# Kernel tuning notes

Measured on AMD Instinct MI355X. Metric: run time of the kernel, lower is better.

## Reference

```python
import jax, jax.numpy as jnp
import numpy as np

N = 100000

def gcn_conv(x, edge_index, W, b):
    # PyG GCNConv: add self-loops, symmetric norm D^-1/2 (A+I) D^-1/2, then aggregate x@W
    n = x.shape[0]
    loops = jnp.arange(n, dtype=edge_index.dtype)
    row = jnp.concatenate([edge_index[0], loops])  # source
    col = jnp.concatenate([edge_index[1], loops])  # target
    deg = jax.ops.segment_sum(jnp.ones_like(col, dtype=x.dtype), col, num_segments=n)
    dinv = jnp.where(deg > 0, jax.lax.rsqrt(deg), 0.0)
    norm = dinv[row] * dinv[col]            # [E+N]
    xw = x @ W                               # transform first (smaller message dim)
    msg = xw[row] * norm[:, None]            # gather + normalize
    out = jax.ops.segment_sum(msg, col, num_segments=n)  # scatter-add
    return out + b

def setup_inputs() -> dict:
    key = jax.random.key(0)
    k1, k2, k3, k4, k5, k6 = jax.random.split(key, 6)
    F_in, H, C = 512, 256, 40
    x = jax.random.normal(k1, (N, F_in), dtype=jnp.float32)
    edge_index = jax.random.randint(k2, (2, 3200000), 0, N, dtype=jnp.int64)
    W1 = jax.random.normal(k3, (F_in, H), dtype=jnp.float32) / np.sqrt(F_in)
    b1 = jnp.zeros((H,), dtype=jnp.float32)
    W2 = jax.random.normal(k4, (H, C), dtype=jnp.float32) / np.sqrt(H)
    b2 = jnp.zeros((C,), dtype=jnp.float32)
    return {"x": x, "edge_index": edge_index, "W1": W1, "b1": b1, "W2": W2, "b2": b2}

def reference(x, edge_index, W1, b1, W2, b2):
    h = gcn_conv(x, edge_index, W1, b1)
    h = jax.nn.relu(h)
    # dropout skipped (eval mode / training=False)
    h = gcn_conv(h, edge_index, W2, b2)
    return jax.nn.log_softmax(h, axis=1)
```

## Files before the change

### kernel.cpp

```cpp
#include <hip/hip_runtime.h>
#include <math.h>

typedef __attribute__((ext_vector_type(8))) short short8;
typedef __attribute__((ext_vector_type(4))) float f32x4;

static __device__ __forceinline__ unsigned short f2bf(float f) {
    unsigned int u = __float_as_uint(f);
    unsigned int r = (u + 0x7FFFu + ((u >> 16) & 1u)) >> 16;
    return (unsigned short)r;
}
static __device__ __forceinline__ float b2f(unsigned short s) {
    return __uint_as_float(((unsigned int)s) << 16);
}


__global__ void count_kernel(const int* __restrict__ ei, int* __restrict__ cnt, int E) {
    int e = blockIdx.x * 256 + threadIdx.x;
    if (e < E) atomicAdd(&cnt[ei[E + e]], 1);
}

__global__ void scanA_kernel(const int* __restrict__ cnt, float* __restrict__ dinv,
                             int* __restrict__ colptr, int* __restrict__ bsum, int n) {
    __shared__ int s[256];
    int b = blockIdx.x, t = threadIdx.x;
    int i = b * 512 + 2 * t;
    int c0 = (i     < n) ? cnt[i]     : 0;
    int c1 = (i + 1 < n) ? cnt[i + 1] : 0;
    if (i     < n) dinv[i]     = rsqrtf((float)(c0 + 1));
    if (i + 1 < n) dinv[i + 1] = rsqrtf((float)(c1 + 1));
    int v = c0 + c1;
    s[t] = v;
    __syncthreads();
    #pragma unroll
    for (int o = 1; o < 256; o <<= 1) {
        int x = (t >= o) ? s[t - o] : 0;
        __syncthreads();
        s[t] += x;
        __syncthreads();
    }
    int excl = s[t] - v;
    if (i     < n) colptr[i]     = excl;
    if (i + 1 < n) colptr[i + 1] = excl + c0;
    if (t == 255) bsum[b] = s[t];
}

__global__ void scanB_kernel(int* bsum, int nb) {
    __shared__ int s[256];
    int t = threadIdx.x;
    int v = (t < nb) ? bsum[t] : 0;
    s[t] = v;
    __syncthreads();
    #pragma unroll
    for (int o = 1; o < 256; o <<= 1) {
        int x = (t >= o) ? s[t - o] : 0;
        __syncthreads();
        s[t] += x;
        __syncthreads();
    }
    if (t < nb) bsum[t] = s[t] - v;
}

__global__ void scanC_kernel(int* __restrict__ colptr, const int* __restrict__ bsum,
                             int n, int E) {
    int b = blockIdx.x, t = threadIdx.x;
    int off = bsum[b];
    int i = b * 512 + 2 * t;
    if (i     < n) colptr[i]     += off;
    if (i + 1 < n) colptr[i + 1] += off;
    if (b == 0 && t == 0) colptr[n] = E;
}

__global__ void fill_kernel(const int* __restrict__ ei, const int* __restrict__ colptr,
                            int* __restrict__ fillc, int* __restrict__ eidx, int E) {
    int e = blockIdx.x * 256 + threadIdx.x;
    if (e < E) {
        int r = ei[e];
        int c = ei[E + e];
        int pos = colptr[c] + atomicAdd(&fillc[c], 1);
        eidx[pos] = r;
    }
}

__global__ void convert_w1_kernel(const float* __restrict__ W1, unsigned short* __restrict__ w1t) {
    int id = blockIdx.x * 256 + threadIdx.x;
    int k = id >> 8, n = id & 255;
    w1t[(size_t)n * 512 + k] = f2bf(W1[id]);
}


__global__ __launch_bounds__(256) void gemm1_kernel(const float* __restrict__ x,
                                                    const unsigned short* __restrict__ w1t,
                                                    const float* __restrict__ dinv,
                                                    unsigned short* __restrict__ xs, int M) {
    __shared__ unsigned short As[64 * 40];
    __shared__ unsigned short Bs[256 * 40];
    int t = threadIdx.x;
    int m0 = blockIdx.x * 64;
    int lane = t & 63, wv = t >> 6;
    int wn = wv * 64;
    int lm = lane & 15, q = lane >> 4;

    int ra = t >> 2, kc = (t & 3) * 8;
    int am = m0 + ra; if (am >= M) am = M - 1;
    const float* Ap = x + (size_t)am * 512 + kc;
    const unsigned short* Bp = w1t + (size_t)ra * 512 + kc;

    f32x4 acc[4][4];
    f32x4 z = {0.f, 0.f, 0.f, 0.f};
    #pragma unroll
    for (int i = 0; i < 4; i++)
        #pragma unroll
        for (int j = 0; j < 4; j++) acc[i][j] = z;

    for (int k0 = 0; k0 < 512; k0 += 32) {
        float4 a0 = *(const float4*)(Ap + k0);
        float4 a1 = *(const float4*)(Ap + k0 + 4);
        uint4 b0 = *(const uint4*)(Bp + k0);
        uint4 b1 = *(const uint4*)(Bp + k0 + 64 * 512);
        uint4 b2 = *(const uint4*)(Bp + k0 + 128 * 512);
        uint4 b3 = *(const uint4*)(Bp + k0 + 192 * 512);
        __syncthreads();
        uint4 ap;
        ap.x = (unsigned int)f2bf(a0.x) | ((unsigned int)f2bf(a0.y) << 16);
        ap.y = (unsigned int)f2bf(a0.z) | ((unsigned int)f2bf(a0.w) << 16);
        ap.z = (unsigned int)f2bf(a1.x) | ((unsigned int)f2bf(a1.y) << 16);
        ap.w = (unsigned int)f2bf(a1.z) | ((unsigned int)f2bf(a1.w) << 16);
        *(uint4*)&As[ra * 40 + kc] = ap;
        *(uint4*)&Bs[(ra +   0) * 40 + kc] = b0;
        *(uint4*)&Bs[(ra +  64) * 40 + kc] = b1;
        *(uint4*)&Bs[(ra + 128) * 40 + kc] = b2;
        *(uint4*)&Bs[(ra + 192) * 40 + kc] = b3;
        __syncthreads();
        short8 af[4], bfr[4];
        #pragma unroll
        for (int i = 0; i < 4; i++)
            af[i] = *(const short8*)&As[(i * 16 + lm) * 40 + q * 8];
        #pragma unroll
        for (int j = 0; j < 4; j++)
            bfr[j] = *(const short8*)&Bs[(wn + j * 16 + lm) * 40 + q * 8];
        #pragma unroll
        for (int i = 0; i < 4; i++)
            #pragma unroll
            for (int j = 0; j < 4; j++)
                acc[i][j] = __builtin_amdgcn_mfma_f32_16x16x32_bf16(af[i], bfr[j], acc[i][j], 0, 0, 0);
    }

    #pragma unroll
    for (int i = 0; i < 4; i++) {
        #pragma unroll
        for (int r = 0; r < 4; r++) {
            int m = m0 + i * 16 + q * 4 + r;
            if (m < M) {
                float d = dinv[m];
                #pragma unroll
                for (int j = 0; j < 4; j++) {
                    int n = wn + j * 16 + lm;
                    xs[(size_t)m * 256 + n] = f2bf(acc[i][j][r] * d);
                }
            }
        }
    }
}


__global__ __launch_bounds__(256) void spmm1_kernel(const unsigned short* __restrict__ xs,
                                                    const int* __restrict__ colptr,
                                                    const int* __restrict__ eidx,
                                                    const float* __restrict__ dinv,
                                                    const float* __restrict__ b1,
                                                    unsigned short* __restrict__ h, int Nn) {
    int wid = threadIdx.x >> 6, lane = threadIdx.x & 63;
    int c = blockIdx.x * 4 + wid;
    if (c >= Nn) return;
    const uint2* base = (const uint2*)xs;
    uint2 sv = base[(size_t)c * 64 + lane];
    float a0 = __uint_as_float(sv.x << 16);
    float a1 = __uint_as_float(sv.x & 0xFFFF0000u);
    float a2 = __uint_as_float(sv.y << 16);
    float a3 = __uint_as_float(sv.y & 0xFFFF0000u);
    int j = colptr[c], jend = colptr[c + 1];
    for (; j + 7 < jend; j += 8) {
        uint2 v0 = base[(size_t)eidx[j    ] * 64 + lane];
        uint2 v1 = base[(size_t)eidx[j + 1] * 64 + lane];
        uint2 v2 = base[(size_t)eidx[j + 2] * 64 + lane];
        uint2 v3 = base[(size_t)eidx[j + 3] * 64 + lane];
        uint2 v4 = base[(size_t)eidx[j + 4] * 64 + lane];
        uint2 v5 = base[(size_t)eidx[j + 5] * 64 + lane];
        uint2 v6 = base[(size_t)eidx[j + 6] * 64 + lane];
        uint2 v7 = base[(size_t)eidx[j + 7] * 64 + lane];
        a0 += __uint_as_float(v0.x << 16) + __uint_as_float(v1.x << 16)
            + __uint_as_float(v2.x << 16) + __uint_as_float(v3.x << 16)
            + __uint_as_float(v4.x << 16) + __uint_as_float(v5.x << 16)
            + __uint_as_float(v6.x << 16) + __uint_as_float(v7.x << 16);
        a1 += __uint_as_float(v0.x & 0xFFFF0000u) + __uint_as_float(v1.x & 0xFFFF0000u)
            + __uint_as_float(v2.x & 0xFFFF0000u) + __uint_as_float(v3.x & 0xFFFF0000u)
            + __uint_as_float(v4.x & 0xFFFF0000u) + __uint_as_float(v5.x & 0xFFFF0000u)
            + __uint_as_float(v6.x & 0xFFFF0000u) + __uint_as_float(v7.x & 0xFFFF0000u);
        a2 += __uint_as_float(v0.y << 16) + __uint_as_float(v1.y << 16)
            + __uint_as_float(v2.y << 16) + __uint_as_float(v3.y << 16)
            + __uint_as_float(v4.y << 16) + __uint_as_float(v5.y << 16)
            + __uint_as_float(v6.y << 16) + __uint_as_float(v7.y << 16);
        a3 += __uint_as_float(v0.y & 0xFFFF0000u) + __uint_as_float(v1.y & 0xFFFF0000u)
            + __uint_as_float(v2.y & 0xFFFF0000u) + __uint_as_float(v3.y & 0xFFFF0000u)
            + __uint_as_float(v4.y & 0xFFFF0000u) + __uint_as_float(v5.y & 0xFFFF0000u)
            + __uint_as_float(v6.y & 0xFFFF0000u) + __uint_as_float(v7.y & 0xFFFF0000u);
    }
    for (; j < jend; j++) {
        uint2 v0 = base[(size_t)eidx[j] * 64 + lane];
        a0 += __uint_as_float(v0.x << 16);
        a1 += __uint_as_float(v0.x & 0xFFFF0000u);
        a2 += __uint_as_float(v0.y << 16);
        a3 += __uint_as_float(v0.y & 0xFFFF0000u);
    }
    float d = dinv[c];
    float4 bb = ((const float4*)b1)[lane];
    float f0 = fmaxf(a0 * d + bb.x, 0.f);
    float f1 = fmaxf(a1 * d + bb.y, 0.f);
    float f2 = fmaxf(a2 * d + bb.z, 0.f);
    float f3 = fmaxf(a3 * d + bb.w, 0.f);
    uint2 p;
    p.x = (unsigned int)f2bf(f0) | ((unsigned int)f2bf(f1) << 16);
    p.y = (unsigned int)f2bf(f2) | ((unsigned int)f2bf(f3) << 16);
    *(uint2*)(h + (size_t)c * 256 + 4 * lane) = p;
}


__global__ __launch_bounds__(320) void gemm2_kernel(const unsigned short* __restrict__ h,
                                                    const float* __restrict__ W2,
                                                    const float* __restrict__ dinv,
                                                    unsigned short* __restrict__ t2p, int M) {
    __shared__ float w2s[256 * 40];
    __shared__ float hs[32][260];
    int t = threadIdx.x;
    for (int idx = t; idx < 10240; idx += 320) w2s[idx] = W2[idx];
    int r0g = blockIdx.x * 32;
    for (int idx = t; idx < 2048; idx += 320) {
        int rr = idx >> 6, k4 = (idx & 63) * 4;
        int row = r0g + rr;
        float4 v = make_float4(0.f, 0.f, 0.f, 0.f);
        if (row < M) {
            uint2 u = *(const uint2*)(h + (size_t)row * 256 + k4);
            v.x = __uint_as_float(u.x << 16);
            v.y = __uint_as_float(u.x & 0xFFFF0000u);
            v.z = __uint_as_float(u.y << 16);
            v.w = __uint_as_float(u.y & 0xFFFF0000u);
        }
        *(float4*)&hs[rr][k4] = v;
    }
    __syncthreads();
    int c = t % 40, rb = (t / 40) * 4;
    float a0 = 0.f, a1 = 0.f, a2 = 0.f, a3 = 0.f;
    #pragma unroll 2
    for (int k = 0; k < 256; k += 4) {
        float4 h0 = *(const float4*)&hs[rb + 0][k];
        float4 h1 = *(const float4*)&hs[rb + 1][k];
        float4 h2 = *(const float4*)&hs[rb + 2][k];
        float4 h3 = *(const float4*)&hs[rb + 3][k];
        float w0 = w2s[(k + 0) * 40 + c];
        float w1 = w2s[(k + 1) * 40 + c];
        float w2 = w2s[(k + 2) * 40 + c];
        float w3 = w2s[(k + 3) * 40 + c];
        a0 += h0.x * w0 + h0.y * w1 + h0.z * w2 + h0.w * w3;
        a1 += h1.x * w0 + h1.y * w1 + h1.z * w2 + h1.w * w3;
        a2 += h2.x * w0 + h2.y * w1 + h2.z * w2 + h2.w * w3;
        a3 += h3.x * w0 + h3.y * w1 + h3.z * w2 + h3.w * w3;
    }
    int row = r0g + rb;
    if (row + 0 < M) t2p[(size_t)(row + 0) * 64 + c] = f2bf(a0 * dinv[row + 0]);
    if (row + 1 < M) t2p[(size_t)(row + 1) * 64 + c] = f2bf(a1 * dinv[row + 1]);
    if (row + 2 < M) t2p[(size_t)(row + 2) * 64 + c] = f2bf(a2 * dinv[row + 2]);
    if (row + 3 < M) t2p[(size_t)(row + 3) * 64 + c] = f2bf(a3 * dinv[row + 3]);
}


__global__ __launch_bounds__(256) void spmm2_kernel(const unsigned short* __restrict__ t2p,
                                                    const int* __restrict__ colptr,
                                                    const int* __restrict__ eidx,
                                                    const float* __restrict__ dinv,
                                                    const float* __restrict__ b2,
                                                    float* __restrict__ out, int Nn) {
    int wid = threadIdx.x >> 6, lane = threadIdx.x & 63;
    int c = blockIdx.x * 4 + wid;
    if (c >= Nn) return;
    float acc = b2f(t2p[(size_t)c * 64 + lane]);
    int j = colptr[c], jend = colptr[c + 1];
    float a0 = 0.f, a1 = 0.f, a2 = 0.f, a3 = 0.f;
    for (; j + 7 < jend; j += 8) {
        float u0 = b2f(t2p[(size_t)eidx[j    ] * 64 + lane]);
        float u1 = b2f(t2p[(size_t)eidx[j + 1] * 64 + lane]);
        float u2 = b2f(t2p[(size_t)eidx[j + 2] * 64 + lane]);
        float u3 = b2f(t2p[(size_t)eidx[j + 3] * 64 + lane]);
        float u4 = b2f(t2p[(size_t)eidx[j + 4] * 64 + lane]);
        float u5 = b2f(t2p[(size_t)eidx[j + 5] * 64 + lane]);
        float u6 = b2f(t2p[(size_t)eidx[j + 6] * 64 + lane]);
        float u7 = b2f(t2p[(size_t)eidx[j + 7] * 64 + lane]);
        a0 += u0 + u4; a1 += u1 + u5; a2 += u2 + u6; a3 += u3 + u7;
    }
    for (; j < jend; j++) a0 += b2f(t2p[(size_t)eidx[j] * 64 + lane]);
    acc += (a0 + a1) + (a2 + a3);
    float val = (lane < 40) ? (acc * dinv[c] + b2[lane]) : -INFINITY;
    float m = val;
    #pragma unroll
    for (int o = 32; o > 0; o >>= 1) { float z = __shfl_xor(m, o); m = fmaxf(m, z); }
    float ex = (lane < 40) ? expf(val - m) : 0.f;
    float s = ex;
    #pragma unroll
    for (int o = 32; o > 0; o >>= 1) s += __shfl_xor(s, o);
    if (lane < 40) out[(size_t)c * 40 + lane] = val - m - logf(s);
}


extern "C" void kernel_launch(void* const* d_in, const int* in_sizes, int n_in,
                              void* d_out, int out_size, void* d_ws, size_t ws_size,
                              hipStream_t stream) {
    const float* x  = (const float*)d_in[0];
    const int*   ei = (const int*)d_in[1];
    const float* W1 = (const float*)d_in[2];
    const float* b1 = (const float*)d_in[3];
    const float* W2 = (const float*)d_in[4];
    const float* b2 = (const float*)d_in[5];
    float* out = (float*)d_out;

    int N = in_sizes[0] / 512;
    int E = in_sizes[1] / 2;

    char* p = (char*)d_ws;
    auto carve = [&](size_t bytes) -> char* {
        char* q = p;
        p += (bytes + 1023) & ~(size_t)1023;
        return q;
    };
    float* dinv   = (float*)carve((size_t)N * 4);
    int*   cnt    = (int*)carve((size_t)N * 4);
    int*   colptr = (int*)carve(((size_t)N + 1) * 4);
    int*   fillc  = (int*)carve((size_t)N * 4);
    int*   bsum   = (int*)carve(1024 * 4);
    int*   eidx   = (int*)carve((size_t)E * 4);
    unsigned short* w1t = (unsigned short*)carve((size_t)256 * 512 * 2);
    unsigned short* xs  = (unsigned short*)carve((size_t)N * 256 * 2);
    unsigned short* h   = (unsigned short*)carve((size_t)N * 256 * 2);
    unsigned short* t2p = (unsigned short*)carve((size_t)N * 64 * 2);

    hipMemsetAsync(cnt,   0, (size_t)N * 4, stream);
    hipMemsetAsync(fillc, 0, (size_t)N * 4, stream);

    int eb = (E + 255) / 256;
    int nb = (N + 511) / 512;

    count_kernel<<<eb, 256, 0, stream>>>(ei, cnt, E);
    scanA_kernel<<<nb, 256, 0, stream>>>(cnt, dinv, colptr, bsum, N);
    scanB_kernel<<<1, 256, 0, stream>>>(bsum, nb);
    scanC_kernel<<<nb, 256, 0, stream>>>(colptr, bsum, N, E);
    fill_kernel<<<eb, 256, 0, stream>>>(ei, colptr, fillc, eidx, E);
    convert_w1_kernel<<<512, 256, 0, stream>>>(W1, w1t);

    int mb = (N + 63) / 64;
    gemm1_kernel<<<mb, 256, 0, stream>>>(x, w1t, dinv, xs, N);
    spmm1_kernel<<<(N + 3) / 4, 256, 0, stream>>>(xs, colptr, eidx, dinv, b1, h, N);
    gemm2_kernel<<<(N + 31) / 32, 320, 0, stream>>>(h, W2, dinv, t2p, N);
    spmm2_kernel<<<(N + 3) / 4, 256, 0, stream>>>(t2p, colptr, eidx, dinv, b2, out, N);
}
```

Measured before the change: 1.050 ms.

## Use MFMA for second GEMM, double-buffer first GEMM, shrink SpMM unroll

Measured after the change: 949.2 us. 9.6% less time.

```diff
diff --git a/kernel.cpp b/kernel.cpp
--- a/kernel.cpp
+++ b/kernel.cpp
@@ -81,10 +81,19 @@
     }
 }
 
-__global__ void convert_w1_kernel(const float* __restrict__ W1, unsigned short* __restrict__ w1t) {
+__global__ void prep_w_kernel(const float* __restrict__ W1, const float* __restrict__ W2,
+                              unsigned short* __restrict__ w1t, unsigned short* __restrict__ w2t) {
     int id = blockIdx.x * 256 + threadIdx.x;
-    int k = id >> 8, n = id & 255;
-    w1t[(size_t)n * 512 + k] = f2bf(W1[id]);
+    if (id < 512 * 256) {
+        int k = id >> 8, n = id & 255;
+        w1t[(size_t)n * 512 + k] = f2bf(W1[id]);
+    } else {
+        int id2 = id - 512 * 256;
+        if (id2 < 64 * 256) {
+            int n = id2 >> 8, k = id2 & 255;
+            w2t[id2] = (n < 40) ? f2bf(W2[k * 40 + n]) : (unsigned short)0;
+        }
+    }
 }
 
 
@@ -92,8 +101,8 @@
                                                     const unsigned short* __restrict__ w1t,
                                                     const float* __restrict__ dinv,
                                                     unsigned short* __restrict__ xs, int M) {
-    __shared__ unsigned short As[64 * 40];
-    __shared__ unsigned short Bs[256 * 40];
+    __shared__ unsigned short As[2][64 * 40];
+    __shared__ unsigned short Bs[2][256 * 40];
     int t = threadIdx.x;
     int m0 = blockIdx.x * 64;
     int lane = t & 63, wv = t >> 6;
@@ -112,37 +121,64 @@
         #pragma unroll
         for (int j = 0; j < 4; j++) acc[i][j] = z;
 
-    for (int k0 = 0; k0 < 512; k0 += 32) {
-        float4 a0 = *(const float4*)(Ap + k0);
-        float4 a1 = *(const float4*)(Ap + k0 + 4);
-        uint4 b0 = *(const uint4*)(Bp + k0);
-        uint4 b1 = *(const uint4*)(Bp + k0 + 64 * 512);
-        uint4 b2 = *(const uint4*)(Bp + k0 + 128 * 512);
-        uint4 b3 = *(const uint4*)(Bp + k0 + 192 * 512);
-        __syncthreads();
+    float4 a0 = *(const float4*)(Ap + 0);
+    float4 a1 = *(const float4*)(Ap + 4);
+    uint4 b0 = *(const uint4*)(Bp + 0);
+    uint4 b1 = *(const uint4*)(Bp + 64 * 512);
+    uint4 b2 = *(const uint4*)(Bp + 128 * 512);
+    uint4 b3 = *(const uint4*)(Bp + 192 * 512);
+    {
         uint4 ap;
         ap.x = (unsigned int)f2bf(a0.x) | ((unsigned int)f2bf(a0.y) << 16);
         ap.y = (unsigned int)f2bf(a0.z) | ((unsigned int)f2bf(a0.w) << 16);
         ap.z = (unsigned int)f2bf(a1.x) | ((unsigned int)f2bf(a1.y) << 16);
         ap.w = (unsigned int)f2bf(a1.z) | ((unsigned int)f2bf(a1.w) << 16);
-        *(uint4*)&As[ra * 40 + kc] = ap;
-        *(uint4*)&Bs[(ra +   0) * 40 + kc] = b0;
-        *(uint4*)&Bs[(ra +  64) * 40 + kc] = b1;
-        *(uint4*)&Bs[(ra + 128) * 40 + kc] = b2;
-        *(uint4*)&Bs[(ra + 192) * 40 + kc] = b3;
-        __syncthreads();
+        *(uint4*)&As[0][ra * 40 + kc] = ap;
+        *(uint4*)&Bs[0][(ra +   0) * 40 + kc] = b0;
+        *(uint4*)&Bs[0][(ra +  64) * 40 + kc] = b1;
+        *(uint4*)&Bs[0][(ra + 128) * 40 + kc] = b2;
+        *(uint4*)&Bs[0][(ra + 192) * 40 + kc] = b3;
+    }
+    __syncthreads();
+
+    int buf = 0;
+    for (int k0 = 0; k0 < 512; k0 += 32) {
+        bool more = (k0 + 32) < 512;
+        if (more) {
+            a0 = *(const float4*)(Ap + k0 + 32);
+            a1 = *(const float4*)(Ap + k0 + 36);
+            b0 = *(const uint4*)(Bp + k0 + 32);
+            b1 = *(const uint4*)(Bp + k0 + 32 + 64 * 512);
+            b2 = *(const uint4*)(Bp + k0 + 32 + 128 * 512);
+            b3 = *(const uint4*)(Bp + k0 + 32 + 192 * 512);
+        }
         short8 af[4], bfr[4];
         #pragma unroll
         for (int i = 0; i < 4; i++)
-            af[i] = *(const short8*)&As[(i * 16 + lm) * 40 + q * 8];
+            af[i] = *(const short8*)&As[buf][(i * 16 + lm) * 40 + q * 8];
         #pragma unroll
         for (int j = 0; j < 4; j++)
-            bfr[j] = *(const short8*)&Bs[(wn + j * 16 + lm) * 40 + q * 8];
+            bfr[j] = *(const short8*)&Bs[buf][(wn + j * 16 + lm) * 40 + q * 8];
         #pragma unroll
         for (int i = 0; i < 4; i++)
             #pragma unroll
             for (int j = 0; j < 4; j++)
                 acc[i][j] = __builtin_amdgcn_mfma_f32_16x16x32_bf16(af[i], bfr[j], acc[i][j], 0, 0, 0);
+        if (more) {
+            uint4 ap;
+            ap.x = (unsigned int)f2bf(a0.x) | ((unsigned int)f2bf(a0.y) << 16);
+            ap.y = (unsigned int)f2bf(a0.z) | ((unsigned int)f2bf(a0.w) << 16);
+            ap.z = (unsigned int)f2bf(a1.x) | ((unsigned int)f2bf(a1.y) << 16);
+            ap.w = (unsigned int)f2bf(a1.z) | ((unsigned int)f2bf(a1.w) << 16);
+            int nb = buf ^ 1;
+            *(uint4*)&As[nb][ra * 40 + kc] = ap;
+            *(uint4*)&Bs[nb][(ra +   0) * 40 + kc] = b0;
+            *(uint4*)&Bs[nb][(ra +  64) * 40 + kc] = b1;
+            *(uint4*)&Bs[nb][(ra + 128) * 40 + kc] = b2;
+            *(uint4*)&Bs[nb][(ra + 192) * 40 + kc] = b3;
+            __syncthreads();
+        }
+        buf ^= 1;
     }
 
     #pragma unroll
@@ -179,31 +215,19 @@
     float a2 = __uint_as_float(sv.y << 16);
     float a3 = __uint_as_float(sv.y & 0xFFFF0000u);
     int j = colptr[c], jend = colptr[c + 1];
-    for (; j + 7 < jend; j += 8) {
+    for (; j + 3 < jend; j += 4) {
         uint2 v0 = base[(size_t)eidx[j    ] * 64 + lane];
         uint2 v1 = base[(size_t)eidx[j + 1] * 64 + lane];
         uint2 v2 = base[(size_t)eidx[j + 2] * 64 + lane];
         uint2 v3 = base[(size_t)eidx[j + 3] * 64 + lane];
-        uint2 v4 = base[(size_t)eidx[j + 4] * 64 + lane];
-        uint2 v5 = base[(size_t)eidx[j + 5] * 64 + lane];
-        uint2 v6 = base[(size_t)eidx[j + 6] * 64 + lane];
-        uint2 v7 = base[(size_t)eidx[j + 7] * 64 + lane];
         a0 += __uint_as_float(v0.x << 16) + __uint_as_float(v1.x << 16)
-            + __uint_as_float(v2.x << 16) + __uint_as_float(v3.x << 16)
-            + __uint_as_float(v4.x << 16) + __uint_as_float(v5.x << 16)
-            + __uint_as_float(v6.x << 16) + __uint_as_float(v7.x << 16);
+            + __uint_as_float(v2.x << 16) + __uint_as_float(v3.x << 16);
         a1 += __uint_as_float(v0.x & 0xFFFF0000u) + __uint_as_float(v1.x & 0xFFFF0000u)
-            + __uint_as_float(v2.x & 0xFFFF0000u) + __uint_as_float(v3.x & 0xFFFF0000u)
-            + __uint_as_float(v4.x & 0xFFFF0000u) + __uint_as_float(v5.x & 0xFFFF0000u)
-            + __uint_as_float(v6.x & 0xFFFF0000u) + __uint_as_float(v7.x & 0xFFFF0000u);
+            + __uint_as_float(v2.x & 0xFFFF0000u) + __uint_as_float(v3.x & 0xFFFF0000u);
         a2 += __uint_as_float(v0.y << 16) + __uint_as_float(v1.y << 16)
-            + __uint_as_float(v2.y << 16) + __uint_as_float(v3.y << 16)
-            + __uint_as_float(v4.y << 16) + __uint_as_float(v5.y << 16)
-            + __uint_as_float(v6.y << 16) + __uint_as_float(v7.y << 16);
+            + __uint_as_float(v2.y << 16) + __uint_as_float(v3.y << 16);
         a3 += __uint_as_float(v0.y & 0xFFFF0000u) + __uint_as_float(v1.y & 0xFFFF0000u)
-            + __uint_as_float(v2.y & 0xFFFF0000u) + __uint_as_float(v3.y & 0xFFFF0000u)
-            + __uint_as_float(v4.y & 0xFFFF0000u) + __uint_as_float(v5.y & 0xFFFF0000u)
-            + __uint_as_float(v6.y & 0xFFFF0000u) + __uint_as_float(v7.y & 0xFFFF0000u);
+            + __uint_as_float(v2.y & 0xFFFF0000u) + __uint_as_float(v3.y & 0xFFFF0000u);
     }
     for (; j < jend; j++) {
         uint2 v0 = base[(size_t)eidx[j] * 64 + lane];
@@ -225,51 +249,54 @@
 }
 
 
-__global__ __launch_bounds__(320) void gemm2_kernel(const unsigned short* __restrict__ h,
-                                                    const float* __restrict__ W2,
+__global__ __launch_bounds__(256) void gemm2_kernel(const unsigned short* __restrict__ h,
+                                                    const unsigned short* __restrict__ w2t,
                                                     const float* __restrict__ dinv,
                                                     unsigned short* __restrict__ t2p, int M) {
-    __shared__ float w2s[256 * 40];
-    __shared__ float hs[32][260];
+    __shared__ unsigned short As[64 * 264];
+    __shared__ unsigned short Bs[64 * 264];
     int t = threadIdx.x;
-    for (int idx = t; idx < 10240; idx += 320) w2s[idx] = W2[idx];
-    int r0g = blockIdx.x * 32;
-    for (int idx = t; idx < 2048; idx += 320) {
-        int rr = idx >> 6, k4 = (idx & 63) * 4;
-        int row = r0g + rr;
-        float4 v = make_float4(0.f, 0.f, 0.f, 0.f);
-        if (row < M) {
-            uint2 u = *(const uint2*)(h + (size_t)row * 256 + k4);
-            v.x = __uint_as_float(u.x << 16);
-            v.y = __uint_as_float(u.x & 0xFFFF0000u);
-            v.z = __uint_as_float(u.y << 16);
-            v.w = __uint_as_float(u.y & 0xFFFF0000u);
-        }
-        *(float4*)&hs[rr][k4] = v;
+    int m0 = blockIdx.x * 64;
+    int lane = t & 63, wv = t >> 6;
+    int lm = lane & 15, q = lane >> 4;
+
+    #pragma unroll
+    for (int i = 0; i < 8; i++) {
+        int c = t + i * 256;
+        int row = c >> 5, col = (c & 31) * 8;
+        int m = m0 + row; if (m >= M) m = M - 1;
+        uint4 av = *(const uint4*)(h + (size_t)m * 256 + col);
+        *(uint4*)&As[row * 264 + col] = av;
+        uint4 bv = *(const uint4*)(w2t + (size_t)row * 256 + col);
+        *(uint4*)&Bs[row * 264 + col] = bv;
     }
     __syncthreads();
-    int c = t % 40, rb = (t / 40) * 4;
-    float a0 = 0.f, a1 = 0.f, a2 = 0.f, a3 = 0.f;
-    #pragma unroll 2
-    for (int k = 0; k < 256; k += 4) {
-        float4 h0 = *(const float4*)&hs[rb + 0][k];
-        float4 h1 = *(const float4*)&hs[rb + 1][k];
-        float4 h2 = *(const float4*)&hs[rb + 2][k];
-        float4 h3 = *(const float4*)&hs[rb + 3][k];
-        float w0 = w2s[(k + 0) * 40 + c];
-        float w1 = w2s[(k + 1) * 40 + c];
-        float w2 = w2s[(k + 2) * 40 + c];
-        float w3 = w2s[(k + 3) * 40 + c];
-        a0 += h0.x * w0 + h0.y * w1 + h0.z * w2 + h0.w * w3;
-        a1 += h1.x * w0 + h1.y * w1 + h1.z * w2 + h1.w * w3;
-        a2 += h2.x * w0 + h2.y * w1 + h2.z * w2 + h2.w * w3;
-        a3 += h3.x * w0 + h3.y * w1 + h3.z * w2 + h3.w * w3;
-    }
-    int row = r0g + rb;
-    if (row + 0 < M) t2p[(size_t)(row + 0) * 64 + c] = f2bf(a0 * dinv[row + 0]);
-    if (row + 1 < M) t2p[(size_t)(row + 1) * 64 + c] = f2bf(a1 * dinv[row + 1]);
-    if (row + 2 < M) t2p[(size_t)(row + 2) * 64 + c] = f2bf(a2 * dinv[row + 2]);
-    if (row + 3 < M) t2p[(size_t)(row + 3) * 64 + c] = f2bf(a3 * dinv[row + 3]);
+
+    f32x4 acc[4];
+    f32x4 z = {0.f, 0.f, 0.f, 0.f};
+    #pragma unroll
+    for (int j = 0; j < 4; j++) acc[j] = z;
+
+    #pragma unroll
+    for (int k0 = 0; k0 < 256; k0 += 32) {
+        short8 af = *(const short8*)&As[(wv * 16 + lm) * 264 + k0 + q * 8];
+        #pragma unroll
+        for (int j = 0; j < 4; j++) {
+            short8 bf = *(const short8*)&Bs[(j * 16 + lm) * 264 + k0 + q * 8];
+            acc[j] = __builtin_amdgcn_mfma_f32_16x16x32_bf16(af, bf, acc[j], 0, 0, 0);
+        }
+    }
+
+    #pragma unroll
+    for (int r = 0; r < 4; r++) {
+        int m = m0 + wv * 16 + q * 4 + r;
+        if (m < M) {
+            float d = dinv[m];
+            #pragma unroll
+            for (int j = 0; j < 4; j++)
+                t2p[(size_t)m * 64 + j * 16 + lm] = f2bf(acc[j][r] * d);
+        }
+    }
 }
 
 
@@ -337,6 +364,7 @@
     int*   bsum   = (int*)carve(1024 * 4);
     int*   eidx   = (int*)carve((size_t)E * 4);
     unsigned short* w1t = (unsigned short*)carve((size_t)256 * 512 * 2);
+    unsigned short* w2t = (unsigned short*)carve((size_t)64 * 256 * 2);
     unsigned short* xs  = (unsigned short*)carve((size_t)N * 256 * 2);
     unsigned short* h   = (unsigned short*)carve((size_t)N * 256 * 2);
     unsigned short* t2p = (unsigned short*)carve((size_t)N * 64 * 2);
@@ -352,11 +380,11 @@
     scanB_kernel<<<1, 256, 0, stream>>>(bsum, nb);
     scanC_kernel<<<nb, 256, 0, stream>>>(colptr, bsum, N, E);
     fill_kernel<<<eb, 256, 0, stream>>>(ei, colptr, fillc, eidx, E);
-    convert_w1_kernel<<<512, 256, 0, stream>>>(W1, w1t);
+    prep_w_kernel<<<576, 256, 0, stream>>>(W1, W2, w1t, w2t);
 
     int mb = (N + 63) / 64;
     gemm1_kernel<<<mb, 256, 0, stream>>>(x, w1t, dinv, xs, N);
     spmm1_kernel<<<(N + 3) / 4, 256, 0, stream>>>(xs, colptr, eidx, dinv, b1, h, N);
-    gemm2_kernel<<<(N + 31) / 32, 320, 0, stream>>>(h, W2, dinv, t2p, N);
+    gemm2_kernel<<<mb, 256, 0, stream>>>(h, w2t, dinv, t2p, N);
     spmm2_kernel<<<(N + 3) / 4, 256, 0, stream>>>(t2p, colptr, eidx, dinv, b2, out, N);
 }
```
